# Kernel optimization log

Measured on AMD Instinct MI355X. Metric: run time of the kernel, lower is better.

The kernel has to match this reference:

```python
import jax, jax.numpy as jnp
import numpy as np


def setup_inputs() -> dict:
    key = jax.random.key(0)
    k1, k2 = jax.random.split(key)
    B, C, h, w = 8, 128, 56, 56
    query_feature = jax.random.normal(k1, (B, C, h, w), dtype=jnp.float32)
    support_feature = jax.random.normal(k2, (B, C, h, w), dtype=jnp.float32)
    return {"query_feature": query_feature, "support_feature": support_feature}


def reference(query_feature, support_feature):
    q, s = query_feature, support_feature
    B, C, h, w = support_feature.shape
    N = h * w
    # torch .view semantics == row-major reshape (NOT a transpose)
    qf = jnp.reshape(query_feature, (B, N, C))      # [B, N, C]
    sf = jnp.reshape(support_feature, (B, C, N))    # [B, C, N]
    batch_adj = jnp.einsum('bnc,bcm->bnm', qf, sf)  # [B, N, N]
    attn = jax.nn.softmax(batch_adj, axis=-1)
    query_logits = jnp.einsum('bnm,bmc->bnc', attn, qf)          # [B, N, C]
    attention_mask = jax.nn.sigmoid(jnp.sum(batch_adj, axis=-1)) # [B, N]
    query_logits = query_logits * attention_mask[..., None]
    sf2 = jnp.reshape(support_feature, (B, N, C))   # another raw view
    support_logits = sf2 * attention_mask[..., None]
    query_logits = jnp.reshape(query_logits, (B, C, h, w))
    support_logits = jnp.reshape(support_logits, (B, C, h, w))
    return (q + query_logits, s + support_logits)
```

## Files before the change

### kernel.cpp

```cpp
#include <hip/hip_runtime.h>
#include <math.h>

#define B_ 8
#define C_ 128
#define N_ 3136
#define MT 64
#define QTBIG 128
#define TILES 49
#define QTILES 25
#define SPLIT0 25

typedef short bf16x8 __attribute__((ext_vector_type(8)));
typedef float f32x4 __attribute__((ext_vector_type(4)));

__device__ __forceinline__ unsigned short f2bf(float f) {
    union { float f; unsigned u; } x; x.f = f;
    return (unsigned short)((x.u + 0x8000u) >> 16);
}

__device__ __forceinline__ void gl_lds16(const void* g, void* l) {
    __builtin_amdgcn_global_load_lds(
        (const __attribute__((address_space(1))) unsigned int*)g,
        (__attribute__((address_space(3))) unsigned int*)l, 16, 0, 0);
}

__global__ __launch_bounds__(256) void colsum_kernel(const float* __restrict__ s,
                                                     float* __restrict__ csum) {
    int blk = blockIdx.x;
    const float* p = s + (size_t)blk * N_;
    float acc = 0.f;
    for (int i = threadIdx.x; i < N_; i += 256) acc += p[i];
#pragma unroll
    for (int off = 32; off > 0; off >>= 1) acc += __shfl_down(acc, off, 64);
    __shared__ float part[4];
    if ((threadIdx.x & 63) == 0) part[threadIdx.x >> 6] = acc;
    __syncthreads();
    if (threadIdx.x == 0) csum[blk] = part[0] + part[1] + part[2] + part[3];
}

__global__ __launch_bounds__(256) void prep_kernel(const float* __restrict__ q,
                                                   const float* __restrict__ s,
                                                   unsigned short* __restrict__ sfT,
                                                   unsigned short* __restrict__ qfT) {
    __shared__ unsigned short T[8448];
    const int tid = threadIdx.x, bid = blockIdx.x;
    const int b = bid & 7, m0 = (bid >> 3) * 64;
    const float* sb = s + (size_t)b * C_ * N_;
    const float* qb = q + (size_t)b * C_ * N_;

    unsigned short (*TA)[132] = (unsigned short (*)[132])T;
#pragma unroll
    for (int st = 0; st < 8; ++st) {
        int idx = st * 256 + tid;
        int c = idx >> 4, m4 = (idx & 15) * 4;
        float4 v = *(const float4*)&sb[(size_t)c * N_ + m0 + m4];
        TA[m4 + 0][c] = f2bf(v.x);
        TA[m4 + 1][c] = f2bf(v.y);
        TA[m4 + 2][c] = f2bf(v.z);
        TA[m4 + 3][c] = f2bf(v.w);
    }
    __syncthreads();
    {
        unsigned short* dst = sfT + (size_t)b * N_ * C_;
#pragma unroll
        for (int st = 0; st < 4; ++st) {
            int g = st * 256 + tid;
            int mr = g >> 4, p = g & 15;
            int lch = p ^ (mr & 15);
            const unsigned short* src = &TA[mr][lch * 8];
            ushort4 a = *(const ushort4*)src;
            ushort4 bq = *(const ushort4*)(src + 4);
            uint4 w;
            w.x = a.x | ((unsigned)a.y << 16);   w.y = a.z | ((unsigned)a.w << 16);
            w.z = bq.x | ((unsigned)bq.y << 16); w.w = bq.z | ((unsigned)bq.w << 16);
            *(uint4*)&dst[(size_t)(m0 + mr) * C_ + p * 8] = w;
        }
    }
    __syncthreads();

    unsigned short (*TB)[66] = (unsigned short (*)[66])T;
#pragma unroll
    for (int st = 0; st < 8; ++st) {
        int idx = st * 256 + tid;
        int r = idx >> 5, c4 = (idx & 31) * 4;
        float4 v = *(const float4*)&qb[(size_t)(m0 + r) * C_ + c4];
        TB[c4 + 0][r] = f2bf(v.x);
        TB[c4 + 1][r] = f2bf(v.y);
        TB[c4 + 2][r] = f2bf(v.z);
        TB[c4 + 3][r] = f2bf(v.w);
    }
    __syncthreads();
    {
        unsigned short* dst = qfT + (size_t)b * C_ * N_;
#pragma unroll
        for (int st = 0; st < 4; ++st) {
            int g = st * 256 + tid;
            int c = g >> 3, p = g & 7;
            int lch = p ^ (c & 7);
            const unsigned short* src = &TB[c][lch * 8];
            ushort2 a0 = *(const ushort2*)(src);
            ushort2 a1 = *(const ushort2*)(src + 2);
            ushort2 a2 = *(const ushort2*)(src + 4);
            ushort2 a3 = *(const ushort2*)(src + 6);
            uint4 w;
            w.x = a0.x | ((unsigned)a0.y << 16); w.y = a1.x | ((unsigned)a1.y << 16);
            w.z = a2.x | ((unsigned)a2.y << 16); w.w = a3.x | ((unsigned)a3.y << 16);
            *(uint4*)&dst[(size_t)c * N_ + m0 + p * 8] = w;
        }
    }
}

__global__ __launch_bounds__(256, 2) void fused_split_kernel(
    const float* __restrict__ q,
    const unsigned short* __restrict__ sfT,
    const unsigned short* __restrict__ qfT,
    float* __restrict__ Opart, float* __restrict__ dpart) {

    __shared__ __align__(16) unsigned short Kb[2][MT * C_];
    __shared__ __align__(16) unsigned short Vb[2][C_ * MT];

    const int tid = threadIdx.x;
    const int lane = tid & 63;
    const int wave = tid >> 6;
    const int l15 = lane & 15;
    const int quad = lane >> 4;
    const int bid = blockIdx.x;
    const int b = bid & 7;
    const int rest = bid >> 3;
    const int qt = rest % QTILES;
    const int split = rest / QTILES;
    const int n0 = qt * QTBIG;
    const int t0 = split ? SPLIT0 : 0;
    const int t1 = split ? TILES : SPLIT0;

    const float* qb = q + (size_t)b * C_ * N_;
    const unsigned short* sfTb = sfT + (size_t)b * N_ * C_;
    const unsigned short* qfTb = qfT + (size_t)b * C_ * N_;

    const int sig_base = ((l15 >> 2) << 3) + (l15 & 3);

    {
        const size_t m1 = (size_t)t0 * MT;
#pragma unroll
        for (int st = 0; st < 4; ++st) {
            int i = st * 256 + tid;
            gl_lds16(sfTb + (m1 + (i >> 4)) * C_ + (i & 15) * 8,
                     &Kb[0][(st * 256 + wave * 64) * 8]);
            gl_lds16(qfTb + (size_t)(i >> 3) * N_ + m1 + (i & 7) * 8,
                     &Vb[0][(st * 256 + wave * 64) * 8]);
        }
    }

    bf16x8 qa[2][4];
#pragma unroll
    for (int rt = 0; rt < 2; ++rt) {
        int grow = n0 + wave * 32 + rt * 16 + l15;
        if (grow > N_ - 1) grow = N_ - 1;
#pragma unroll
        for (int ks = 0; ks < 4; ++ks) {
            int c0 = ks * 32 + quad * 8;
            float4 f0 = *(const float4*)&qb[(size_t)grow * C_ + c0];
            float4 f1 = *(const float4*)&qb[(size_t)grow * C_ + c0 + 4];
            union { unsigned short u[8]; bf16x8 v; } t;
            t.u[0] = f2bf(f0.x); t.u[1] = f2bf(f0.y);
            t.u[2] = f2bf(f0.z); t.u[3] = f2bf(f0.w);
            t.u[4] = f2bf(f1.x); t.u[5] = f2bf(f1.y);
            t.u[6] = f2bf(f1.z); t.u[7] = f2bf(f1.w);
            qa[rt][ks] = t.v;
        }
    }

    f32x4 O[2][8];
#pragma unroll
    for (int rt = 0; rt < 2; ++rt)
#pragma unroll
        for (int nt = 0; nt < 8; ++nt) O[rt][nt] = (f32x4){0.f, 0.f, 0.f, 0.f};
    float dsum[2] = {0.f, 0.f};

    const int ntiles = t1 - t0;
    for (int tt = 0; tt < ntiles; ++tt) {
        const int cur = tt & 1;
        __syncthreads();

        if (tt + 1 < ntiles) {
            const int nxt = cur ^ 1;
            const size_t m1 = (size_t)(t0 + tt + 1) * MT;
#pragma unroll
            for (int st = 0; st < 4; ++st) {
                int i = st * 256 + tid;
                gl_lds16(sfTb + (m1 + (i >> 4)) * C_ + (i & 15) * 8,
                         &Kb[nxt][(st * 256 + wave * 64) * 8]);
                gl_lds16(qfTb + (size_t)(i >> 3) * N_ + m1 + (i & 7) * 8,
                         &Vb[nxt][(st * 256 + wave * 64) * 8]);
            }
        }

        f32x4 acc[4][2];
#pragma unroll
        for (int ct = 0; ct < 4; ++ct) {
            acc[ct][0] = (f32x4){0.f, 0.f, 0.f, 0.f};
            acc[ct][1] = (f32x4){0.f, 0.f, 0.f, 0.f};
            const int mrow = sig_base + ((ct & 1) << 2) + ((ct >> 1) << 5);
#pragma unroll
            for (int ks = 0; ks < 4; ++ks) {
                int ch = (ks * 4 + quad) ^ (mrow & 15);
                bf16x8 af = *(const bf16x8*)&Kb[cur][mrow * C_ + ch * 8];
                acc[ct][0] = __builtin_amdgcn_mfma_f32_16x16x32_bf16(af, qa[0][ks], acc[ct][0], 0, 0, 0);
                acc[ct][1] = __builtin_amdgcn_mfma_f32_16x16x32_bf16(af, qa[1][ks], acc[ct][1], 0, 0, 0);
            }
        }

        bf16x8 pa[2][2];
#pragma unroll
        for (int k2 = 0; k2 < 2; ++k2)
#pragma unroll
            for (int rt = 0; rt < 2; ++rt) {
                float e0 = __expf(acc[2 * k2 + 0][rt][0]);
                float e1 = __expf(acc[2 * k2 + 0][rt][1]);
                float e2 = __expf(acc[2 * k2 + 0][rt][2]);
                float e3 = __expf(acc[2 * k2 + 0][rt][3]);
                float e4 = __expf(acc[2 * k2 + 1][rt][0]);
                float e5 = __expf(acc[2 * k2 + 1][rt][1]);
                float e6 = __expf(acc[2 * k2 + 1][rt][2]);
                float e7 = __expf(acc[2 * k2 + 1][rt][3]);
                dsum[rt] += ((e0 + e1) + (e2 + e3)) + ((e4 + e5) + (e6 + e7));
                union { unsigned short u[8]; bf16x8 v; } pk;
                pk.u[0] = f2bf(e0); pk.u[1] = f2bf(e1);
                pk.u[2] = f2bf(e2); pk.u[3] = f2bf(e3);
                pk.u[4] = f2bf(e4); pk.u[5] = f2bf(e5);
                pk.u[6] = f2bf(e6); pk.u[7] = f2bf(e7);
                pa[rt][k2] = pk.v;
            }

#pragma unroll
        for (int k2 = 0; k2 < 2; ++k2)
#pragma unroll
            for (int nt = 0; nt < 8; ++nt) {
                const int crow = nt * 16 + l15;
                int ch = (k2 * 4 + quad) ^ (crow & 7);
                bf16x8 vf = *(const bf16x8*)&Vb[cur][crow * MT + ch * 8];
                O[0][nt] = __builtin_amdgcn_mfma_f32_16x16x32_bf16(pa[0][k2], vf, O[0][nt], 0, 0, 0);
                O[1][nt] = __builtin_amdgcn_mfma_f32_16x16x32_bf16(pa[1][k2], vf, O[1][nt], 0, 0, 0);
            }
    }

#pragma unroll
    for (int rt = 0; rt < 2; ++rt) {
        float d = dsum[rt];
        d += __shfl_xor(d, 16, 64);
        d += __shfl_xor(d, 32, 64);
        if (quad == 0) {
            int grow = n0 + wave * 32 + rt * 16 + l15;
            if (grow < N_)
                dpart[(size_t)(split * 8 + b) * N_ + grow] = d;
        }
    }

#pragma unroll
    for (int rt = 0; rt < 2; ++rt)
#pragma unroll
        for (int r = 0; r < 4; ++r) {
            int grow = n0 + wave * 32 + rt * 16 + quad * 4 + r;
            if (grow < N_) {
                float* dst = Opart + ((size_t)(split * 8 + b) * N_ + grow) * C_;
#pragma unroll
                for (int nt = 0; nt < 8; ++nt)
                    dst[nt * 16 + l15] = O[rt][nt][r];
            }
        }
}

__global__ __launch_bounds__(256) void combine_kernel(
    const float* __restrict__ q, const float* __restrict__ s,
    const float* __restrict__ csum, const float* __restrict__ Opart,
    const float* __restrict__ dpart,
    float* __restrict__ out0, float* __restrict__ out1) {

    __shared__ float cs[C_];
    const int tid = threadIdx.x, bid = blockIdx.x;
    const int b = bid & 7, r0 = (bid >> 3) * 32;
    if (tid < C_) cs[tid] = csum[b * C_ + tid];
    __syncthreads();

    const int lane = tid & 63, wave = tid >> 6;
    const int row_l = wave * 8 + (lane >> 3);
    const int j = lane & 7;
    const int grow = r0 + row_l;
    const size_t base = (size_t)b * N_ * C_ + (size_t)grow * C_;

    float4 qv[4];
    float dot = 0.f;
#pragma unroll
    for (int k = 0; k < 4; ++k) {
        int c = k * 32 + j * 4;
        qv[k] = *(const float4*)&q[base + c];
        dot += qv[k].x * cs[c] + qv[k].y * cs[c + 1] +
               qv[k].z * cs[c + 2] + qv[k].w * cs[c + 3];
    }
    dot += __shfl_xor(dot, 1, 64);
    dot += __shfl_xor(dot, 2, 64);
    dot += __shfl_xor(dot, 4, 64);
    const float mask = 1.0f / (1.0f + __expf(-dot));

    const float dtot = dpart[(size_t)b * N_ + grow] +
                       dpart[(size_t)(8 + b) * N_ + grow];
    const float scl = mask / dtot;
    const float om = 1.0f + mask;

    const size_t p0 = ((size_t)b * N_ + grow) * C_;
    const size_t p1 = p0 + (size_t)8 * N_ * C_;
#pragma unroll
    for (int k = 0; k < 4; ++k) {
        int c = k * 32 + j * 4;
        float4 oa = *(const float4*)&Opart[p0 + c];
        float4 ob = *(const float4*)&Opart[p1 + c];
        float4 sv = *(const float4*)&s[base + c];
        float4 r0v, r1v;
        r0v.x = qv[k].x + (oa.x + ob.x) * scl;
        r0v.y = qv[k].y + (oa.y + ob.y) * scl;
        r0v.z = qv[k].z + (oa.z + ob.z) * scl;
        r0v.w = qv[k].w + (oa.w + ob.w) * scl;
        r1v.x = sv.x * om; r1v.y = sv.y * om;
        r1v.z = sv.z * om; r1v.w = sv.w * om;
        *(float4*)&out0[base + c] = r0v;
        *(float4*)&out1[base + c] = r1v;
    }
}

__global__ __launch_bounds__(256, 2) void fused_kernel(const float* __restrict__ q,
                                                       const float* __restrict__ s,
                                                       const float* __restrict__ csum,
                                                       float* __restrict__ out0,
                                                       float* __restrict__ out1) {
    __shared__ float QtT[C_][68];
    __shared__ float Kt[C_ * 32];
    __shared__ float Vt[32 * C_];
    __shared__ float PT[32][68];
    __shared__ float mask_l[64];
    __shared__ float csum_l[C_];

    const int t = threadIdx.x;
    const int l = t & 63, w = t >> 6, tx = t & 15, ty = t >> 4;
    const int bid = blockIdx.x, b = bid & 7, n0 = (bid >> 3) * 64;
    const float* qb = q + (size_t)b * C_ * N_;
    const float* sb = s + (size_t)b * C_ * N_;

#pragma unroll
    for (int jj = 0; jj < 2; ++jj) {
        int c = l + 64 * jj;
#pragma unroll
        for (int i = 0; i < 16; ++i) QtT[c][w + 4 * i] = qb[(size_t)(n0 + w + 4 * i) * C_ + c];
    }
    if (t < C_) csum_l[t] = csum[b * C_ + t];
    __syncthreads();
    if (t < 64) {
        float d = 0.f;
        for (int c = 0; c < C_; ++c) d += QtT[c][t] * csum_l[c];
        mask_l[t] = 1.0f / (1.0f + __expf(-d));
    }
    float4 Oa[4], Ob[4];
#pragma unroll
    for (int i = 0; i < 4; ++i) { Oa[i] = make_float4(0,0,0,0); Ob[i] = make_float4(0,0,0,0); }
    float m_r[4], l_r[4];
#pragma unroll
    for (int i = 0; i < 4; ++i) { m_r[i] = -3.0e38f; l_r[i] = 0.f; }

    for (int mt = 0; mt < N_ / 32; ++mt) {
        const int m0 = mt * 32;
        __syncthreads();
#pragma unroll
        for (int i = 0; i < 4; ++i) {
            int s4 = (w * 4 + i) * 64 + l;
            int c = s4 >> 3, mq = (s4 & 7) * 4;
            *(float4*)&Kt[c * 32 + mq] = *(const float4*)&sb[(size_t)c * N_ + m0 + mq];
            *(float4*)&Vt[s4 * 4] = *(const float4*)&qb[(size_t)m0 * C_ + s4 * 4];
        }
        __syncthreads();
        float a[4][2];
#pragma unroll
        for (int i = 0; i < 4; ++i) a[i][0] = a[i][1] = 0.f;
#pragma unroll 4
        for (int k = 0; k < C_; ++k) {
            const float4 qv = *(const float4*)&QtT[k][4 * ty];
            const float2 kv = *(const float2*)&Kt[k * 32 + 2 * tx];
            a[0][0] = fmaf(qv.x, kv.x, a[0][0]); a[0][1] = fmaf(qv.x, kv.y, a[0][1]);
            a[1][0] = fmaf(qv.y, kv.x, a[1][0]); a[1][1] = fmaf(qv.y, kv.y, a[1][1]);
            a[2][0] = fmaf(qv.z, kv.x, a[2][0]); a[2][1] = fmaf(qv.z, kv.y, a[2][1]);
            a[3][0] = fmaf(qv.w, kv.x, a[3][0]); a[3][1] = fmaf(qv.w, kv.y, a[3][1]);
        }
#pragma unroll
        for (int i = 0; i < 4; ++i) {
            float tm = fmaxf(a[i][0], a[i][1]);
            tm = fmaxf(tm, __shfl_xor(tm, 1, 64)); tm = fmaxf(tm, __shfl_xor(tm, 2, 64));
            tm = fmaxf(tm, __shfl_xor(tm, 4, 64)); tm = fmaxf(tm, __shfl_xor(tm, 8, 64));
            float nm = fmaxf(m_r[i], tm);
            float al = __expf(m_r[i] - nm);
            m_r[i] = nm;
            float p0 = __expf(a[i][0] - nm), p1 = __expf(a[i][1] - nm);
            float ts = p0 + p1;
            ts += __shfl_xor(ts, 1, 64); ts += __shfl_xor(ts, 2, 64);
            ts += __shfl_xor(ts, 4, 64); ts += __shfl_xor(ts, 8, 64);
            l_r[i] = l_r[i] * al + ts;
            PT[2 * tx + 0][4 * ty + i] = p0;
            PT[2 * tx + 1][4 * ty + i] = p1;
            Oa[i].x *= al; Oa[i].y *= al; Oa[i].z *= al; Oa[i].w *= al;
            Ob[i].x *= al; Ob[i].y *= al; Ob[i].z *= al; Ob[i].w *= al;
        }
        __syncthreads();
#pragma unroll 2
        for (int j = 0; j < 32; ++j) {
            const float4 pv = *(const float4*)&PT[j][4 * ty];
            const float4 v0 = *(const float4*)&Vt[j * C_ + 4 * tx];
            const float4 v1 = *(const float4*)&Vt[j * C_ + 4 * tx + 64];
            Oa[0].x = fmaf(pv.x, v0.x, Oa[0].x); Oa[0].y = fmaf(pv.x, v0.y, Oa[0].y);
            Oa[0].z = fmaf(pv.x, v0.z, Oa[0].z); Oa[0].w = fmaf(pv.x, v0.w, Oa[0].w);
            Ob[0].x = fmaf(pv.x, v1.x, Ob[0].x); Ob[0].y = fmaf(pv.x, v1.y, Ob[0].y);
            Ob[0].z = fmaf(pv.x, v1.z, Ob[0].z); Ob[0].w = fmaf(pv.x, v1.w, Ob[0].w);
            Oa[1].x = fmaf(pv.y, v0.x, Oa[1].x); Oa[1].y = fmaf(pv.y, v0.y, Oa[1].y);
            Oa[1].z = fmaf(pv.y, v0.z, Oa[1].z); Oa[1].w = fmaf(pv.y, v0.w, Oa[1].w);
            Ob[1].x = fmaf(pv.y, v1.x, Ob[1].x); Ob[1].y = fmaf(pv.y, v1.y, Ob[1].y);
            Ob[1].z = fmaf(pv.y, v1.z, Ob[1].z); Ob[1].w = fmaf(pv.y, v1.w, Ob[1].w);
            Oa[2].x = fmaf(pv.z, v0.x, Oa[2].x); Oa[2].y = fmaf(pv.z, v0.y, Oa[2].y);
            Oa[2].z = fmaf(pv.z, v0.z, Oa[2].z); Oa[2].w = fmaf(pv.z, v0.w, Oa[2].w);
            Ob[2].x = fmaf(pv.z, v1.x, Ob[2].x); Ob[2].y = fmaf(pv.z, v1.y, Ob[2].y);
            Ob[2].z = fmaf(pv.z, v1.z, Ob[2].z); Ob[2].w = fmaf(pv.z, v1.w, Ob[2].w);
            Oa[3].x = fmaf(pv.w, v0.x, Oa[3].x); Oa[3].y = fmaf(pv.w, v0.y, Oa[3].y);
            Oa[3].z = fmaf(pv.w, v0.z, Oa[3].z); Oa[3].w = fmaf(pv.w, v0.w, Oa[3].w);
            Ob[3].x = fmaf(pv.w, v1.x, Ob[3].x); Ob[3].y = fmaf(pv.w, v1.y, Ob[3].y);
            Ob[3].z = fmaf(pv.w, v1.z, Ob[3].z); Ob[3].w = fmaf(pv.w, v1.w, Ob[3].w);
        }
    }
#pragma unroll
    for (int i = 0; i < 4; ++i) {
        const int r = 4 * ty + i;
        const float mk = mask_l[r];
        const float scl = mk / l_r[i];
        const float om = 1.0f + mk;
        const size_t row = (size_t)b * C_ * N_ + (size_t)(n0 + r) * C_;
#pragma unroll
        for (int h = 0; h < 2; ++h) {
            const int c = 4 * tx + 64 * h;
            const float4 ov = h ? Ob[i] : Oa[i];
            float4 qv = *(const float4*)&qb[(size_t)(n0 + r) * C_ + c];
            float4 sv = *(const float4*)&sb[(size_t)(n0 + r) * C_ + c];
            float4 o0, o1;
            o0.x = qv.x + ov.x * scl; o0.y = qv.y + ov.y * scl;
            o0.z = qv.z + ov.z * scl; o0.w = qv.w + ov.w * scl;
            o1.x = sv.x * om; o1.y = sv.y * om; o1.z = sv.z * om; o1.w = sv.w * om;
            *(float4*)&out0[row + c] = o0;
            *(float4*)&out1[row + c] = o1;
        }
    }
}

extern "C" void kernel_launch(void* const* d_in, const int* in_sizes, int n_in,
                              void* d_out, int out_size, void* d_ws, size_t ws_size,
                              hipStream_t stream) {
    const float* q = (const float*)d_in[0];
    const float* s = (const float*)d_in[1];
    float* out0 = (float*)d_out;
    float* out1 = out0 + (size_t)B_ * C_ * N_;
    float* csum = (float*)d_ws;

    const size_t elems = (size_t)B_ * N_ * C_;
    const size_t need = 4096
                      + 2 * elems * sizeof(unsigned short)
                      + 2 * elems * sizeof(float)
                      + 2 * (size_t)B_ * N_ * sizeof(float);

    colsum_kernel<<<B_ * C_, 256, 0, stream>>>(s, csum);
    if (ws_size >= need) {
        unsigned short* sfT = (unsigned short*)((char*)d_ws + 4096);
        unsigned short* qfT = sfT + elems;
        float* Opart = (float*)(qfT + elems);
        float* dpart = Opart + 2 * elems;
        prep_kernel<<<B_ * TILES, 256, 0, stream>>>(q, s, sfT, qfT);
        fused_split_kernel<<<2 * QTILES * B_, 256, 0, stream>>>(q, sfT, qfT, Opart, dpart);
        combine_kernel<<<B_ * (N_ / 32), 256, 0, stream>>>(q, s, csum, Opart, dpart, out0, out1);
    } else {
        fused_kernel<<<B_ * (N_ / 64), 256, 0, stream>>>(q, s, csum, out0, out1);
    }
}
```

Before: 150.0 us.

## Split key range four ways with smaller tiles, bf16 partials, and MFMA priority

Halves the key tile to 32 rows and splits the key range into four chunks, so the attention kernel launches twice as many blocks at higher occupancy (launch bounds 4). The V operand is re-laid out in prep as tile-contiguous chunks, which lets loads be linear, and the K swizzle is adjusted. Partial outputs are stored as bf16 to cut workspace traffic, and the combine kernel sums four partials. MFMA sections get raised wave priority. The risks are lower precision in the partials and more combine reads.

```diff
diff --git a/kernel.cpp b/kernel.cpp
--- a/kernel.cpp
+++ b/kernel.cpp
@@ -4,11 +4,11 @@
 #define B_ 8
 #define C_ 128
 #define N_ 3136
-#define MT 64
+#define MT 32
+#define TILES 98
 #define QTBIG 128
-#define TILES 49
 #define QTILES 25
-#define SPLIT0 25
+#define SPLITS 4
 
 typedef short bf16x8 __attribute__((ext_vector_type(8)));
 typedef float f32x4 __attribute__((ext_vector_type(4)));
@@ -16,6 +16,10 @@
 __device__ __forceinline__ unsigned short f2bf(float f) {
     union { float f; unsigned u; } x; x.f = f;
     return (unsigned short)((x.u + 0x8000u) >> 16);
+}
+
+__device__ __forceinline__ float bf2f(unsigned short h) {
+    union { unsigned u; float f; } x; x.u = (unsigned)h << 16; return x.f;
 }
 
 __device__ __forceinline__ void gl_lds16(const void* g, void* l) {
@@ -66,7 +70,8 @@
         for (int st = 0; st < 4; ++st) {
             int g = st * 256 + tid;
             int mr = g >> 4, p = g & 15;
-            int lch = p ^ (mr & 15);
+            int sw = (mr & 15) ^ ((mr >> 1) & 4);
+            int lch = p ^ sw;
             const unsigned short* src = &TA[mr][lch * 8];
             ushort4 a = *(const ushort4*)src;
             ushort4 bq = *(const ushort4*)(src + 4);
@@ -91,13 +96,13 @@
     }
     __syncthreads();
     {
-        unsigned short* dst = qfT + (size_t)b * C_ * N_;
+        unsigned short* dstb = qfT + (size_t)b * N_ * C_;
 #pragma unroll
         for (int st = 0; st < 4; ++st) {
             int g = st * 256 + tid;
-            int c = g >> 3, p = g & 7;
-            int lch = p ^ (c & 7);
-            const unsigned short* src = &TB[c][lch * 8];
+            int p = g >> 7, c = g & 127;
+            int t = (m0 >> 5) + (p >> 2), ch = p & 3;
+            const unsigned short* src = &TB[c][p * 8];
             ushort2 a0 = *(const ushort2*)(src);
             ushort2 a1 = *(const ushort2*)(src + 2);
             ushort2 a2 = *(const ushort2*)(src + 4);
@@ -105,19 +110,19 @@
             uint4 w;
             w.x = a0.x | ((unsigned)a0.y << 16); w.y = a1.x | ((unsigned)a1.y << 16);
             w.z = a2.x | ((unsigned)a2.y << 16); w.w = a3.x | ((unsigned)a3.y << 16);
-            *(uint4*)&dst[(size_t)c * N_ + m0 + p * 8] = w;
-        }
-    }
-}
-
-__global__ __launch_bounds__(256, 2) void fused_split_kernel(
+            *(uint4*)&dstb[((size_t)t * 4 + ch) * (C_ * 8) + c * 8] = w;
+        }
+    }
+}
+
+__global__ __launch_bounds__(256, 4) void fused_split_kernel(
     const float* __restrict__ q,
     const unsigned short* __restrict__ sfT,
     const unsigned short* __restrict__ qfT,
-    float* __restrict__ Opart, float* __restrict__ dpart) {
+    unsigned short* __restrict__ Opart, float* __restrict__ dpart) {
 
     __shared__ __align__(16) unsigned short Kb[2][MT * C_];
-    __shared__ __align__(16) unsigned short Vb[2][C_ * MT];
+    __shared__ __align__(16) unsigned short Vb[2][MT * C_];
 
     const int tid = threadIdx.x;
     const int lane = tid & 63;
@@ -130,23 +135,23 @@
     const int qt = rest % QTILES;
     const int split = rest / QTILES;
     const int n0 = qt * QTBIG;
-    const int t0 = split ? SPLIT0 : 0;
-    const int t1 = split ? TILES : SPLIT0;
+    const int t0 = split * 24 + (split < 2 ? split : 2);
+    const int ntiles = (split < 2) ? 25 : 24;
 
     const float* qb = q + (size_t)b * C_ * N_;
     const unsigned short* sfTb = sfT + (size_t)b * N_ * C_;
-    const unsigned short* qfTb = qfT + (size_t)b * C_ * N_;
+    const unsigned short* qfTb = qfT + (size_t)b * N_ * C_;
 
     const int sig_base = ((l15 >> 2) << 3) + (l15 & 3);
 
     {
         const size_t m1 = (size_t)t0 * MT;
 #pragma unroll
-        for (int st = 0; st < 4; ++st) {
+        for (int st = 0; st < 2; ++st) {
             int i = st * 256 + tid;
             gl_lds16(sfTb + (m1 + (i >> 4)) * C_ + (i & 15) * 8,
                      &Kb[0][(st * 256 + wave * 64) * 8]);
-            gl_lds16(qfTb + (size_t)(i >> 3) * N_ + m1 + (i & 7) * 8,
+            gl_lds16(qfTb + (size_t)t0 * (MT * C_) + (size_t)i * 8,
                      &Vb[0][(st * 256 + wave * 64) * 8]);
         }
     }
@@ -177,7 +182,6 @@
         for (int nt = 0; nt < 8; ++nt) O[rt][nt] = (f32x4){0.f, 0.f, 0.f, 0.f};
     float dsum[2] = {0.f, 0.f};
 
-    const int ntiles = t1 - t0;
     for (int tt = 0; tt < ntiles; ++tt) {
         const int cur = tt & 1;
         __syncthreads();
@@ -186,62 +190,61 @@
             const int nxt = cur ^ 1;
             const size_t m1 = (size_t)(t0 + tt + 1) * MT;
 #pragma unroll
-            for (int st = 0; st < 4; ++st) {
+            for (int st = 0; st < 2; ++st) {
                 int i = st * 256 + tid;
                 gl_lds16(sfTb + (m1 + (i >> 4)) * C_ + (i & 15) * 8,
                          &Kb[nxt][(st * 256 + wave * 64) * 8]);
-                gl_lds16(qfTb + (size_t)(i >> 3) * N_ + m1 + (i & 7) * 8,
+                gl_lds16(qfTb + (size_t)(t0 + tt + 1) * (MT * C_) + (size_t)i * 8,
                          &Vb[nxt][(st * 256 + wave * 64) * 8]);
             }
         }
 
-        f32x4 acc[4][2];
-#pragma unroll
-        for (int ct = 0; ct < 4; ++ct) {
+        f32x4 acc[2][2];
+        __builtin_amdgcn_s_setprio(1);
+#pragma unroll
+        for (int ct = 0; ct < 2; ++ct) {
             acc[ct][0] = (f32x4){0.f, 0.f, 0.f, 0.f};
             acc[ct][1] = (f32x4){0.f, 0.f, 0.f, 0.f};
-            const int mrow = sig_base + ((ct & 1) << 2) + ((ct >> 1) << 5);
+            const int mrow = sig_base + (ct << 2);
+            const int sw = (mrow & 15) ^ ((mrow >> 1) & 4);
 #pragma unroll
             for (int ks = 0; ks < 4; ++ks) {
-                int ch = (ks * 4 + quad) ^ (mrow & 15);
+                int ch = (ks * 4 + quad) ^ sw;
                 bf16x8 af = *(const bf16x8*)&Kb[cur][mrow * C_ + ch * 8];
                 acc[ct][0] = __builtin_amdgcn_mfma_f32_16x16x32_bf16(af, qa[0][ks], acc[ct][0], 0, 0, 0);
                 acc[ct][1] = __builtin_amdgcn_mfma_f32_16x16x32_bf16(af, qa[1][ks], acc[ct][1], 0, 0, 0);
             }
         }
-
-        bf16x8 pa[2][2];
-#pragma unroll
-        for (int k2 = 0; k2 < 2; ++k2)
-#pragma unroll
-            for (int rt = 0; rt < 2; ++rt) {
-                float e0 = __expf(acc[2 * k2 + 0][rt][0]);
-                float e1 = __expf(acc[2 * k2 + 0][rt][1]);
-                float e2 = __expf(acc[2 * k2 + 0][rt][2]);
-                float e3 = __expf(acc[2 * k2 + 0][rt][3]);
-                float e4 = __expf(acc[2 * k2 + 1][rt][0]);
-                float e5 = __expf(acc[2 * k2 + 1][rt][1]);
-                float e6 = __expf(acc[2 * k2 + 1][rt][2]);
-                float e7 = __expf(acc[2 * k2 + 1][rt][3]);
-                dsum[rt] += ((e0 + e1) + (e2 + e3)) + ((e4 + e5) + (e6 + e7));
-                union { unsigned short u[8]; bf16x8 v; } pk;
-                pk.u[0] = f2bf(e0); pk.u[1] = f2bf(e1);
-                pk.u[2] = f2bf(e2); pk.u[3] = f2bf(e3);
-                pk.u[4] = f2bf(e4); pk.u[5] = f2bf(e5);
-                pk.u[6] = f2bf(e6); pk.u[7] = f2bf(e7);
-                pa[rt][k2] = pk.v;
-            }
-
-#pragma unroll
-        for (int k2 = 0; k2 < 2; ++k2)
-#pragma unroll
-            for (int nt = 0; nt < 8; ++nt) {
-                const int crow = nt * 16 + l15;
-                int ch = (k2 * 4 + quad) ^ (crow & 7);
-                bf16x8 vf = *(const bf16x8*)&Vb[cur][crow * MT + ch * 8];
-                O[0][nt] = __builtin_amdgcn_mfma_f32_16x16x32_bf16(pa[0][k2], vf, O[0][nt], 0, 0, 0);
-                O[1][nt] = __builtin_amdgcn_mfma_f32_16x16x32_bf16(pa[1][k2], vf, O[1][nt], 0, 0, 0);
-            }
+        __builtin_amdgcn_s_setprio(0);
+
+        bf16x8 pa[2];
+#pragma unroll
+        for (int rt = 0; rt < 2; ++rt) {
+            float e0 = __expf(acc[0][rt][0]);
+            float e1 = __expf(acc[0][rt][1]);
+            float e2 = __expf(acc[0][rt][2]);
+            float e3 = __expf(acc[0][rt][3]);
+            float e4 = __expf(acc[1][rt][0]);
+            float e5 = __expf(acc[1][rt][1]);
+            float e6 = __expf(acc[1][rt][2]);
+            float e7 = __expf(acc[1][rt][3]);
+            dsum[rt] += ((e0 + e1) + (e2 + e3)) + ((e4 + e5) + (e6 + e7));
+            union { unsigned short u[8]; bf16x8 v; } pk;
+            pk.u[0] = f2bf(e0); pk.u[1] = f2bf(e1);
+            pk.u[2] = f2bf(e2); pk.u[3] = f2bf(e3);
+            pk.u[4] = f2bf(e4); pk.u[5] = f2bf(e5);
+            pk.u[6] = f2bf(e6); pk.u[7] = f2bf(e7);
+            pa[rt] = pk.v;
+        }
+
+        __builtin_amdgcn_s_setprio(1);
+#pragma unroll
+        for (int nt = 0; nt < 8; ++nt) {
+            bf16x8 vf = *(const bf16x8*)&Vb[cur][quad * (C_ * 8) + (nt * 16 + l15) * 8];
+            O[0][nt] = __builtin_amdgcn_mfma_f32_16x16x32_bf16(pa[0], vf, O[0][nt], 0, 0, 0);
+            O[1][nt] = __builtin_amdgcn_mfma_f32_16x16x32_bf16(pa[1], vf, O[1][nt], 0, 0, 0);
+        }
+        __builtin_amdgcn_s_setprio(0);
     }
 
 #pragma unroll
@@ -262,17 +265,17 @@
         for (int r = 0; r < 4; ++r) {
             int grow = n0 + wave * 32 + rt * 16 + quad * 4 + r;
             if (grow < N_) {
-                float* dst = Opart + ((size_t)(split * 8 + b) * N_ + grow) * C_;
+                unsigned short* dst = Opart + ((size_t)(split * 8 + b) * N_ + grow) * C_;
 #pragma unroll
                 for (int nt = 0; nt < 8; ++nt)
-                    dst[nt * 16 + l15] = O[rt][nt][r];
+                    dst[nt * 16 + l15] = f2bf(O[rt][nt][r]);
             }
         }
 }
 
 __global__ __launch_bounds__(256) void combine_kernel(
     const float* __restrict__ q, const float* __restrict__ s,
-    const float* __restrict__ csum, const float* __restrict__ Opart,
+    const float* __restrict__ csum, const unsigned short* __restrict__ Opart,
     const float* __restrict__ dpart,
     float* __restrict__ out0, float* __restrict__ out1) {
 
@@ -302,24 +305,29 @@
     dot += __shfl_xor(dot, 4, 64);
     const float mask = 1.0f / (1.0f + __expf(-dot));
 
-    const float dtot = dpart[(size_t)b * N_ + grow] +
-                       dpart[(size_t)(8 + b) * N_ + grow];
+    float dtot = 0.f;
+#pragma unroll
+    for (int sp = 0; sp < SPLITS; ++sp)
+        dtot += dpart[(size_t)(sp * 8 + b) * N_ + grow];
     const float scl = mask / dtot;
     const float om = 1.0f + mask;
 
-    const size_t p0 = ((size_t)b * N_ + grow) * C_;
-    const size_t p1 = p0 + (size_t)8 * N_ * C_;
 #pragma unroll
     for (int k = 0; k < 4; ++k) {
         int c = k * 32 + j * 4;
-        float4 oa = *(const float4*)&Opart[p0 + c];
-        float4 ob = *(const float4*)&Opart[p1 + c];
+        float osx = 0.f, osy = 0.f, osz = 0.f, osw = 0.f;
+#pragma unroll
+        for (int sp = 0; sp < SPLITS; ++sp) {
+            const ushort4 ov = *(const ushort4*)&Opart[((size_t)(sp * 8 + b) * N_ + grow) * C_ + c];
+            osx += bf2f(ov.x); osy += bf2f(ov.y);
+            osz += bf2f(ov.z); osw += bf2f(ov.w);
+        }
         float4 sv = *(const float4*)&s[base + c];
         float4 r0v, r1v;
-        r0v.x = qv[k].x + (oa.x + ob.x) * scl;
-        r0v.y = qv[k].y + (oa.y + ob.y) * scl;
-        r0v.z = qv[k].z + (oa.z + ob.z) * scl;
-        r0v.w = qv[k].w + (oa.w + ob.w) * scl;
+        r0v.x = qv[k].x + osx * scl;
+        r0v.y = qv[k].y + osy * scl;
+        r0v.z = qv[k].z + osz * scl;
+        r0v.w = qv[k].w + osw * scl;
         r1v.x = sv.x * om; r1v.y = sv.y * om;
         r1v.z = sv.z * om; r1v.w = sv.w * om;
         *(float4*)&out0[base + c] = r0v;
@@ -465,17 +473,17 @@
     const size_t elems = (size_t)B_ * N_ * C_;
     const size_t need = 4096
                       + 2 * elems * sizeof(unsigned short)
-                      + 2 * elems * sizeof(float)
-                      + 2 * (size_t)B_ * N_ * sizeof(float);
+                      + (size_t)SPLITS * elems * sizeof(unsigned short)
+                      + (size_t)SPLITS * B_ * N_ * sizeof(float);
 
     colsum_kernel<<<B_ * C_, 256, 0, stream>>>(s, csum);
     if (ws_size >= need) {
         unsigned short* sfT = (unsigned short*)((char*)d_ws + 4096);
         unsigned short* qfT = sfT + elems;
-        float* Opart = (float*)(qfT + elems);
-        float* dpart = Opart + 2 * elems;
-        prep_kernel<<<B_ * TILES, 256, 0, stream>>>(q, s, sfT, qfT);
-        fused_split_kernel<<<2 * QTILES * B_, 256, 0, stream>>>(q, sfT, qfT, Opart, dpart);
+        unsigned short* Opart = qfT + elems;
+        float* dpart = (float*)(Opart + (size_t)SPLITS * elems);
+        prep_kernel<<<B_ * (N_ / 64), 256, 0, stream>>>(q, s, sfT, qfT);
+        fused_split_kernel<<<SPLITS * QTILES * B_, 256, 0, stream>>>(q, sfT, qfT, Opart, dpart);
         combine_kernel<<<B_ * (N_ / 32), 256, 0, stream>>>(q, s, csum, Opart, dpart, out0, out1);
     } else {
         fused_kernel<<<B_ * (N_ / 64), 256, 0, stream>>>(q, s, csum, out0, out1);
```

Measured after the change: 193.1 us. 1.29x slower.
